# Optimization experiments

Hardware: AMD Instinct MI355X
Metric: run time of the kernel (lower is better)

Reference implementation:

```python
import jax, jax.numpy as jnp
import numpy as np

N_NODES = 50000
N_EDGES = 600000
F_IN = 128
DIM_H = 256
N_CLASSES = 40
BN_EPS = 1e-5


def setup_inputs() -> dict:
    key = jax.random.key(0)
    ks = jax.random.split(key, 10)
    x = jax.random.normal(ks[0], (N_NODES, F_IN), dtype=jnp.float32)
    edge_index = jax.random.randint(ks[1], (2, N_EDGES), 0, N_NODES, dtype=jnp.int64)
    s1 = 1.0 / np.sqrt(F_IN)
    s2 = 1.0 / np.sqrt(DIM_H)
    W1 = jax.random.uniform(ks[2], (F_IN, DIM_H), jnp.float32, -s1, s1)
    b1 = jax.random.uniform(ks[3], (DIM_H,), jnp.float32, -s1, s1)
    gamma = jnp.ones((DIM_H,), jnp.float32)
    beta = jnp.zeros((DIM_H,), jnp.float32)
    W2 = jax.random.uniform(ks[4], (DIM_H, DIM_H), jnp.float32, -s2, s2)
    b2 = jax.random.uniform(ks[5], (DIM_H,), jnp.float32, -s2, s2)
    Wlin = jax.random.uniform(ks[6], (DIM_H, N_CLASSES), jnp.float32, -s2, s2)
    blin = jax.random.uniform(ks[7], (N_CLASSES,), jnp.float32, -s2, s2)
    return {"x": x, "edge_index": edge_index, "W1": W1, "b1": b1,
            "gamma": gamma, "beta": beta, "W2": W2, "b2": b2,
            "Wlin": Wlin, "blin": blin}


def reference(x, edge_index, W1, b1, gamma, beta, W2, b2, Wlin, blin):
    src, dst = edge_index[0], edge_index[1]
    # GIN sum aggregation: agg[i] = sum_{(j->i)} x[j]; eps = 0 (default)
    agg = jax.ops.segment_sum(x[src], dst, num_segments=N_NODES)  # [N, F_IN]
    h = x + agg
    # MLP: Linear -> BatchNorm1d (training-mode batch stats) -> ReLU -> Linear -> ReLU
    h = h @ W1 + b1                               # [N, DIM_H]
    mean = jnp.mean(h, axis=0)
    var = jnp.var(h, axis=0)                      # biased, as torch BN uses for normalization
    h = (h - mean) * jax.lax.rsqrt(var + BN_EPS) * gamma + beta
    h = jax.nn.relu(h)
    h = jax.nn.relu(h @ W2 + b2)                  # MLP final ReLU; outer x.relu() is idempotent
    return h @ Wlin + blin                        # [N, N_CLASSES]
```

## Files before the change

### kernel.cpp

```cpp
#include <hip/hip_runtime.h>

#define F_IN 128
#define DIM_H 256
#define N_CLASSES 40
#define BN_EPS 1e-5f
#define M_PAD 50176

typedef short bf16x8 __attribute__((ext_vector_type(8)));
typedef float f32x4 __attribute__((ext_vector_type(4)));

__device__ __forceinline__ unsigned short f2bf(float f) {
    union { float f; unsigned u; } v; v.f = f;
    unsigned r = v.u + 0x7fff + ((v.u >> 16) & 1);
    return (unsigned short)(r >> 16);
}
__device__ __forceinline__ float bf2f(unsigned short u) {
    union { unsigned u; float f; } v; v.u = ((unsigned)u) << 16;
    return v.f;
}
__device__ __forceinline__ float4 bf2f4(ushort4 u) {
    return make_float4(bf2f(u.x), bf2f(u.y), bf2f(u.z), bf2f(u.w));
}

__global__ void hist_kernel(const int* __restrict__ dst, int* __restrict__ hist, int nE) {
    int e = blockIdx.x * blockDim.x + threadIdx.x;
    if (e >= nE) return;
    atomicAdd(&hist[dst[e]], 1);
}

__global__ void scan_blocks_kernel(const int* __restrict__ hist,
                                   int* __restrict__ blockSums, int M) {
    __shared__ int lds[256];
    int t = threadIdx.x;
    int i = blockIdx.x * 256 + t;
    lds[t] = (i < M) ? hist[i] : 0;
    __syncthreads();
    for (int off = 128; off > 0; off >>= 1) {
        if (t < off) lds[t] += lds[t + off];
        __syncthreads();
    }
    if (t == 0) blockSums[blockIdx.x] = lds[0];
}

__global__ void scan_final_kernel(const int* __restrict__ hist,
                                  const int* __restrict__ blockSums,
                                  int* __restrict__ start, int M, int nE) {
    __shared__ int lds[256];
    int t = threadIdx.x;
    lds[t] = (t < blockIdx.x) ? blockSums[t] : 0;
    __syncthreads();
    for (int o = 128; o > 0; o >>= 1) {
        if (t < o) lds[t] += lds[t + o];
        __syncthreads();
    }
    int off = lds[0];
    __syncthreads();
    int i = blockIdx.x * 256 + t;
    int orig = (i < M) ? hist[i] : 0;
    lds[t] = orig;
    __syncthreads();
    for (int o = 1; o < 256; o <<= 1) {
        int v = (t >= o) ? lds[t - o] : 0;
        __syncthreads();
        lds[t] += v;
        __syncthreads();
    }
    if (i < M) start[i] = off + lds[t] - orig;
    if (blockIdx.x == 0 && t == 0) start[M] = nE;
}

__global__ void fill_kernel(const int* __restrict__ src, const int* __restrict__ dst,
                            const int* __restrict__ start, int* __restrict__ cursor,
                            int* __restrict__ order, int nE) {
    int e = blockIdx.x * blockDim.x + threadIdx.x;
    if (e >= nE) return;
    int d = dst[e];
    int pos = start[d] + atomicAdd(&cursor[d], 1);
    order[pos] = src[e];
}

__global__ void prep_kernel(const float* __restrict__ x, unsigned short* __restrict__ xb,
                            const float* __restrict__ W1, const float* __restrict__ W2,
                            const float* __restrict__ Wl,
                            unsigned short* __restrict__ W1t,
                            unsigned short* __restrict__ W2t,
                            unsigned short* __restrict__ Wlt,
                            int* __restrict__ histz, int XQ, int ZQ) {
    int idx = blockIdx.x * 256 + threadIdx.x;
    if (idx < XQ) {
        float4 v = ((const float4*)x)[idx];
        ushort4 o;
        o.x = f2bf(v.x); o.y = f2bf(v.y); o.z = f2bf(v.z); o.w = f2bf(v.w);
        ((ushort4*)xb)[idx] = o;
        return;
    }
    int j = idx - XQ;
    if (j < 32768) {
        int n = j >> 7, k = j & 127;
        W1t[j] = f2bf(W1[k * DIM_H + n]);
    } else if (j < 32768 + 65536) {
        int i = j - 32768;
        int n = i >> 8, k = i & 255;
        W2t[i] = f2bf(W2[k * DIM_H + n]);
    } else if (j < 32768 + 65536 + 16384) {
        int i = j - 98304;
        int n = i >> 8, k = i & 255;
        Wlt[i] = f2bf((n < N_CLASSES) ? Wl[k * N_CLASSES + n] : 0.f);
    } else {
        int z = j - 114688;
        if (z >= 0 && z < ZQ) ((int4*)histz)[z] = make_int4(0, 0, 0, 0);
    }
}

__global__ void bn_reduce_kernel(const float* __restrict__ partials, int R,
                                 const float* __restrict__ gamma,
                                 const float* __restrict__ beta,
                                 float* __restrict__ scale,
                                 float* __restrict__ shift, int M) {
    __shared__ float ls[256], lss[256];
    int c = blockIdx.x, t = threadIdx.x;
    float s = 0.f, ss = 0.f;
    for (int r = t; r < R; r += 256) {
        s += partials[(long)r * 512 + c];
        ss += partials[(long)r * 512 + 256 + c];
    }
    ls[t] = s; lss[t] = ss;
    __syncthreads();
    for (int o = 128; o > 0; o >>= 1) {
        if (t < o) { ls[t] += ls[t + o]; lss[t] += lss[t + o]; }
        __syncthreads();
    }
    if (t == 0) {
        float inv = 1.0f / (float)M;
        float mean = ls[0] * inv;
        float var = lss[0] * inv - mean * mean;
        float sc = gamma[c] * rsqrtf(var + BN_EPS);
        scale[c] = sc;
        shift[c] = beta[c] - mean * sc;
    }
}

__global__ __launch_bounds__(256) void gather_kernel(
    const unsigned short* __restrict__ xb,
    const int* __restrict__ order, const int* __restrict__ start,
    unsigned short* __restrict__ A1, int M) {
    int node = blockIdx.x * 8 + (threadIdx.x >> 5);
    if (node >= M) return;
    int lane32 = threadIdx.x & 31;
    const ushort4* xv = (const ushort4*)xb;
    float4 a0 = bf2f4(xv[(size_t)node * 32 + lane32]);
    float4 a1 = make_float4(0.f, 0.f, 0.f, 0.f);
    float4 a2 = a1, a3 = a1;
    int e0 = start[node], e1 = start[node + 1];
    int e = e0;
    for (; e + 8 <= e1; e += 8) {
        int s0 = order[e],     s1 = order[e + 1], s2 = order[e + 2], s3 = order[e + 3];
        int s4 = order[e + 4], s5 = order[e + 5], s6 = order[e + 6], s7 = order[e + 7];
        ushort4 u0 = xv[(size_t)s0 * 32 + lane32];
        ushort4 u1 = xv[(size_t)s1 * 32 + lane32];
        ushort4 u2 = xv[(size_t)s2 * 32 + lane32];
        ushort4 u3 = xv[(size_t)s3 * 32 + lane32];
        ushort4 u4 = xv[(size_t)s4 * 32 + lane32];
        ushort4 u5 = xv[(size_t)s5 * 32 + lane32];
        ushort4 u6 = xv[(size_t)s6 * 32 + lane32];
        ushort4 u7 = xv[(size_t)s7 * 32 + lane32];
        float4 v0 = bf2f4(u0), v1 = bf2f4(u1), v2 = bf2f4(u2), v3 = bf2f4(u3);
        float4 v4 = bf2f4(u4), v5 = bf2f4(u5), v6 = bf2f4(u6), v7 = bf2f4(u7);
        a0.x += v0.x; a0.y += v0.y; a0.z += v0.z; a0.w += v0.w;
        a1.x += v1.x; a1.y += v1.y; a1.z += v1.z; a1.w += v1.w;
        a2.x += v2.x; a2.y += v2.y; a2.z += v2.z; a2.w += v2.w;
        a3.x += v3.x; a3.y += v3.y; a3.z += v3.z; a3.w += v3.w;
        a0.x += v4.x; a0.y += v4.y; a0.z += v4.z; a0.w += v4.w;
        a1.x += v5.x; a1.y += v5.y; a1.z += v5.z; a1.w += v5.w;
        a2.x += v6.x; a2.y += v6.y; a2.z += v6.z; a2.w += v6.w;
        a3.x += v7.x; a3.y += v7.y; a3.z += v7.z; a3.w += v7.w;
    }
    for (; e + 4 <= e1; e += 4) {
        int s0 = order[e], s1 = order[e + 1], s2 = order[e + 2], s3 = order[e + 3];
        float4 v0 = bf2f4(xv[(size_t)s0 * 32 + lane32]);
        float4 v1 = bf2f4(xv[(size_t)s1 * 32 + lane32]);
        float4 v2 = bf2f4(xv[(size_t)s2 * 32 + lane32]);
        float4 v3 = bf2f4(xv[(size_t)s3 * 32 + lane32]);
        a0.x += v0.x; a0.y += v0.y; a0.z += v0.z; a0.w += v0.w;
        a1.x += v1.x; a1.y += v1.y; a1.z += v1.z; a1.w += v1.w;
        a2.x += v2.x; a2.y += v2.y; a2.z += v2.z; a2.w += v2.w;
        a3.x += v3.x; a3.y += v3.y; a3.z += v3.z; a3.w += v3.w;
    }
    for (; e < e1; ++e) {
        float4 v = bf2f4(xv[(size_t)order[e] * 32 + lane32]);
        a1.x += v.x; a1.y += v.y; a1.z += v.z; a1.w += v.w;
    }
    float4 t;
    t.x = (a0.x + a1.x) + (a2.x + a3.x);
    t.y = (a0.y + a1.y) + (a2.y + a3.y);
    t.z = (a0.z + a1.z) + (a2.z + a3.z);
    t.w = (a0.w + a1.w) + (a2.w + a3.w);
    ushort4 o;
    o.x = f2bf(t.x); o.y = f2bf(t.y); o.z = f2bf(t.z); o.w = f2bf(t.w);
    ((ushort4*)A1)[(size_t)node * 32 + lane32] = o;
}

__global__ __launch_bounds__(512, 4) void gemm1_kernel(
    const unsigned short* __restrict__ A1, const unsigned short* __restrict__ W1t,
    const float* __restrict__ b1, unsigned short* __restrict__ h1,
    float* __restrict__ partials, int M) {
    constexpr int S = 4;
    constexpr int PA = 40, PB = 40, PH = 264;
    constexpr int STAGE = 128 * PA + 256 * PB;
    __shared__ __align__(16) unsigned short lds[128 * PH];
    unsigned short* h1t = lds;

    int tid = threadIdx.x;
    int wave = tid >> 6, lane = tid & 63;
    int wm = wave >> 2, wn = wave & 3;
    int l15 = lane & 15, q = lane >> 4;
    long row0 = (long)blockIdx.x * 128;

    int am = tid >> 2, ac = tid & 3;
    bf16x8 ar, br[2];
    auto loadAB = [&](int s) {
        ar = *(const bf16x8*)(A1 + (row0 + am) * F_IN + s * 32 + ac * 8);
#pragma unroll
        for (int i = 0; i < 2; ++i) {
            int ch = tid + i * 512;
            int m = ch >> 2, c = ch & 3;
            br[i] = *(const bf16x8*)(W1t + m * F_IN + s * 32 + c * 8);
        }
    };
    auto writeAB = [&](int buf) {
        unsigned short* As = lds + buf * STAGE;
        unsigned short* Bs = As + 128 * PA;
        *(bf16x8*)(&As[am * PA + ac * 8]) = ar;
#pragma unroll
        for (int i = 0; i < 2; ++i) {
            int ch = tid + i * 512;
            int m = ch >> 2, c = ch & 3;
            *(bf16x8*)(&Bs[m * PB + c * 8]) = br[i];
        }
    };

    f32x4 acc[4][4] = {};
    loadAB(0);
    writeAB(0);
#pragma unroll
    for (int s = 0; s < S; ++s) {
        if (s + 1 < S) loadAB(s + 1);
        __syncthreads();
        const unsigned short* As = lds + (s & 1) * STAGE;
        const unsigned short* Bs = As + 128 * PA;
        bf16x8 af[4], bfr[4];
#pragma unroll
        for (int mt = 0; mt < 4; ++mt)
            af[mt] = *(const bf16x8*)(&As[(wm * 64 + mt * 16 + l15) * PA + q * 8]);
#pragma unroll
        for (int nt = 0; nt < 4; ++nt)
            bfr[nt] = *(const bf16x8*)(&Bs[(wn * 64 + nt * 16 + l15) * PB + q * 8]);
#pragma unroll
        for (int mt = 0; mt < 4; ++mt)
#pragma unroll
            for (int nt = 0; nt < 4; ++nt)
                acc[mt][nt] = __builtin_amdgcn_mfma_f32_16x16x32_bf16(
                    af[mt], bfr[nt], acc[mt][nt], 0, 0, 0);
        if (s + 1 < S) writeAB((s + 1) & 1);
    }
    __syncthreads();

#pragma unroll
    for (int nt = 0; nt < 4; ++nt) {
        int col = wn * 64 + nt * 16 + l15;
        float b = b1[col];
        float s = 0.f, ss = 0.f;
#pragma unroll
        for (int mt = 0; mt < 4; ++mt) {
#pragma unroll
            for (int r = 0; r < 4; ++r) {
                long row = row0 + wm * 64 + mt * 16 + q * 4 + r;
                float v = acc[mt][nt][r] + b;
                if (row < M) { s += v; ss += v * v; }
                h1t[(wm * 64 + mt * 16 + q * 4 + r) * PH + col] = f2bf(v);
            }
        }
        s += __shfl_xor(s, 16, 64);  s += __shfl_xor(s, 32, 64);
        ss += __shfl_xor(ss, 16, 64); ss += __shfl_xor(ss, 32, 64);
        if (lane < 16) {
            long pr = (long)blockIdx.x * 2 + wm;
            partials[pr * 512 + col] = s;
            partials[pr * 512 + 256 + col] = ss;
        }
    }
    __syncthreads();
    {
        int srow = tid >> 2, scol = (tid & 3) * 64;
        unsigned short* dst = h1 + (row0 + srow) * DIM_H + scol;
        const unsigned short* srcp = &h1t[srow * PH + scol];
#pragma unroll
        for (int j = 0; j < 8; ++j)
            *(bf16x8*)(dst + j * 8) = *(const bf16x8*)(srcp + j * 8);
    }
}

__global__ __launch_bounds__(512, 4) void gemm23_kernel(
    const unsigned short* __restrict__ h1, const unsigned short* __restrict__ W2t,
    const float* __restrict__ b2,
    const float* __restrict__ scale, const float* __restrict__ shift,
    const unsigned short* __restrict__ Wlt, const float* __restrict__ blin,
    float* __restrict__ out, int M) {
    constexpr int S = 8;
    constexpr int PA = 40, PB = 40, PH = 264;
    constexpr int STAGE = 128 * PA + 256 * PB;
    __shared__ __align__(16) unsigned short lds[128 * PH];
    unsigned short* h2t = lds;

    int tid = threadIdx.x;
    int wave = tid >> 6, lane = tid & 63;
    int wm = wave >> 2, wn = wave & 3;
    int l15 = lane & 15, q = lane >> 4;
    long row0 = (long)blockIdx.x * 128;

    int am = tid >> 2, ac = tid & 3;
    bf16x8 ar, br[2];
    auto loadAB = [&](int s) {
        ar = *(const bf16x8*)(h1 + (row0 + am) * DIM_H + s * 32 + ac * 8);
#pragma unroll
        for (int i = 0; i < 2; ++i) {
            int ch = tid + i * 512;
            int m = ch >> 2, c = ch & 3;
            br[i] = *(const bf16x8*)(W2t + m * DIM_H + s * 32 + c * 8);
        }
    };
    auto writeAB = [&](int s, int buf) {
        unsigned short* As = lds + buf * STAGE;
        unsigned short* Bs = As + 128 * PA;
        {
            int kb = s * 32 + ac * 8;
            float4 sc0 = *(const float4*)(scale + kb);
            float4 sc1 = *(const float4*)(scale + kb + 4);
            float4 sh0 = *(const float4*)(shift + kb);
            float4 sh1 = *(const float4*)(shift + kb + 4);
            float scv[8] = {sc0.x, sc0.y, sc0.z, sc0.w, sc1.x, sc1.y, sc1.z, sc1.w};
            float shv[8] = {sh0.x, sh0.y, sh0.z, sh0.w, sh1.x, sh1.y, sh1.z, sh1.w};
            bf16x8 v = ar;
#pragma unroll
            for (int j = 0; j < 8; ++j) {
                float f = bf2f((unsigned short)v[j]);
                f = fmaxf(f * scv[j] + shv[j], 0.f);
                v[j] = (short)f2bf(f);
            }
            *(bf16x8*)(&As[am * PA + ac * 8]) = v;
        }
#pragma unroll
        for (int i = 0; i < 2; ++i) {
            int ch = tid + i * 512;
            int m = ch >> 2, c = ch & 3;
            *(bf16x8*)(&Bs[m * PB + c * 8]) = br[i];
        }
    };

    f32x4 acc[4][4] = {};
    loadAB(0);
    writeAB(0, 0);
#pragma unroll
    for (int s = 0; s < S; ++s) {
        if (s + 1 < S) loadAB(s + 1);
        __syncthreads();
        const unsigned short* As = lds + (s & 1) * STAGE;
        const unsigned short* Bs = As + 128 * PA;
        bf16x8 af[4], bfr[4];
#pragma unroll
        for (int mt = 0; mt < 4; ++mt)
            af[mt] = *(const bf16x8*)(&As[(wm * 64 + mt * 16 + l15) * PA + q * 8]);
#pragma unroll
        for (int nt = 0; nt < 4; ++nt)
            bfr[nt] = *(const bf16x8*)(&Bs[(wn * 64 + nt * 16 + l15) * PB + q * 8]);
#pragma unroll
        for (int mt = 0; mt < 4; ++mt)
#pragma unroll
            for (int nt = 0; nt < 4; ++nt)
                acc[mt][nt] = __builtin_amdgcn_mfma_f32_16x16x32_bf16(
                    af[mt], bfr[nt], acc[mt][nt], 0, 0, 0);
        if (s + 1 < S) writeAB(s + 1, (s + 1) & 1);
    }
    __syncthreads();

#pragma unroll
    for (int nt = 0; nt < 4; ++nt) {
        int colL = wn * 64 + nt * 16 + l15;
        float b = b2[colL];
#pragma unroll
        for (int mt = 0; mt < 4; ++mt)
#pragma unroll
            for (int r = 0; r < 4; ++r) {
                int rowL = wm * 64 + mt * 16 + q * 4 + r;
                h2t[rowL * PH + colL] = f2bf(fmaxf(acc[mt][nt][r] + b, 0.f));
            }
    }
    __syncthreads();

    f32x4 acc3[3] = {};
#pragma unroll
    for (int s = 0; s < 8; ++s) {
        bf16x8 a3 = *(const bf16x8*)(&h2t[(wave * 16 + l15) * PH + s * 32 + q * 8]);
#pragma unroll
        for (int nt = 0; nt < 3; ++nt) {
            bf16x8 b3 = *(const bf16x8*)(Wlt + (nt * 16 + l15) * 256 + s * 32 + q * 8);
            acc3[nt] = __builtin_amdgcn_mfma_f32_16x16x32_bf16(a3, b3, acc3[nt], 0, 0, 0);
        }
    }
#pragma unroll
    for (int nt = 0; nt < 3; ++nt) {
        int col = nt * 16 + l15;
        if (col < N_CLASSES) {
            float b = blin[col];
#pragma unroll
            for (int r = 0; r < 4; ++r) {
                long row = row0 + wave * 16 + q * 4 + r;
                if (row < M) out[row * N_CLASSES + col] = acc3[nt][r] + b;
            }
        }
    }
}

extern "C" void kernel_launch(void* const* d_in, const int* in_sizes, int n_in,
                              void* d_out, int out_size, void* d_ws, size_t ws_size,
                              hipStream_t stream) {
    const float* x     = (const float*)d_in[0];
    const int*   ei    = (const int*)d_in[1];
    const float* W1    = (const float*)d_in[2];
    const float* b1    = (const float*)d_in[3];
    const float* gamma = (const float*)d_in[4];
    const float* beta  = (const float*)d_in[5];
    const float* W2    = (const float*)d_in[6];
    const float* b2    = (const float*)d_in[7];
    const float* Wlin  = (const float*)d_in[8];
    const float* blin  = (const float*)d_in[9];
    float* out = (float*)d_out;

    int M  = in_sizes[0] / F_IN;
    int nE = in_sizes[1] / 2;
    const int* srcIdx = ei;
    const int* dstIdx = ei + nE;
    int nB = (M + 255) / 256;
    int g128 = (M + 127) / 128;
    int XQ = M * 32;
    int ZQ = 2 * M / 4;

    unsigned short* h1bf  = (unsigned short*)d_ws;
    unsigned short* xb    = h1bf + (size_t)M_PAD * DIM_H;
    unsigned short* A1bf  = xb + (size_t)M_PAD * F_IN;
    unsigned short* W1t   = A1bf + (size_t)M_PAD * F_IN;
    unsigned short* W2t   = W1t + DIM_H * F_IN;
    unsigned short* Wlt   = W2t + DIM_H * DIM_H;
    float*          partials = (float*)(Wlt + 64 * DIM_H);
    float*          scale = partials + (size_t)800 * 512;
    float*          shift = scale + DIM_H;
    int*            hist  = (int*)(shift + DIM_H);
    int*            cursor= hist + M;
    int*            start = cursor + M;
    int*            blockSums = start + (M + 1);
    int*            order = blockSums + 256;

    int tB = 256;
    prep_kernel<<<(XQ + 114688 + ZQ + 255) / 256, 256, 0, stream>>>(
        x, xb, W1, W2, Wlin, W1t, W2t, Wlt, hist, XQ, ZQ);
    hist_kernel<<<(nE + tB - 1) / tB, tB, 0, stream>>>(dstIdx, hist, nE);
    scan_blocks_kernel<<<nB, 256, 0, stream>>>(hist, blockSums, M);
    scan_final_kernel<<<nB, 256, 0, stream>>>(hist, blockSums, start, M, nE);
    fill_kernel<<<(nE + tB - 1) / tB, tB, 0, stream>>>(srcIdx, dstIdx, start, cursor, order, nE);

    gather_kernel<<<(M + 7) / 8, 256, 0, stream>>>(xb, order, start, A1bf, M);
    gemm1_kernel<<<g128, 512, 0, stream>>>(A1bf, W1t, b1, h1bf, partials, M);
    bn_reduce_kernel<<<DIM_H, 256, 0, stream>>>(partials, 2 * g128, gamma, beta, scale, shift, M);
    gemm23_kernel<<<g128, 512, 0, stream>>>(h1bf, W2t, b2, scale, shift, Wlt, blin, out, M);
}
```

Before: 233.6 us.

## Fuse BN reduction into GEMM via atomics and widen gather loads to 16 bytes

Removes the separate bn_reduce kernel. gemm1 now atomically accumulates the per-column sum and sum of squares into a zeroed global buffer, and gemm23 computes scale and shift into shared memory at startup. This saves one launch and the partials round trip, at the cost of atomic contention on 512 addresses and fp32 atomic ordering nondeterminism. Separately, the gather kernel uses 16 lanes per node with 16-byte bf16x8 loads instead of 32 lanes with 8-byte loads, and cuts the accumulators from four to two.

```diff
diff --git a/kernel.cpp b/kernel.cpp
--- a/kernel.cpp
+++ b/kernel.cpp
@@ -17,9 +17,6 @@
 __device__ __forceinline__ float bf2f(unsigned short u) {
     union { unsigned u; float f; } v; v.u = ((unsigned)u) << 16;
     return v.f;
-}
-__device__ __forceinline__ float4 bf2f4(ushort4 u) {
-    return make_float4(bf2f(u.x), bf2f(u.y), bf2f(u.z), bf2f(u.w));
 }
 
 __global__ void hist_kernel(const int* __restrict__ dst, int* __restrict__ hist, int nE) {
@@ -112,98 +109,65 @@
     }
 }
 
-__global__ void bn_reduce_kernel(const float* __restrict__ partials, int R,
-                                 const float* __restrict__ gamma,
-                                 const float* __restrict__ beta,
-                                 float* __restrict__ scale,
-                                 float* __restrict__ shift, int M) {
-    __shared__ float ls[256], lss[256];
-    int c = blockIdx.x, t = threadIdx.x;
-    float s = 0.f, ss = 0.f;
-    for (int r = t; r < R; r += 256) {
-        s += partials[(long)r * 512 + c];
-        ss += partials[(long)r * 512 + 256 + c];
-    }
-    ls[t] = s; lss[t] = ss;
-    __syncthreads();
-    for (int o = 128; o > 0; o >>= 1) {
-        if (t < o) { ls[t] += ls[t + o]; lss[t] += lss[t + o]; }
-        __syncthreads();
-    }
-    if (t == 0) {
-        float inv = 1.0f / (float)M;
-        float mean = ls[0] * inv;
-        float var = lss[0] * inv - mean * mean;
-        float sc = gamma[c] * rsqrtf(var + BN_EPS);
-        scale[c] = sc;
-        shift[c] = beta[c] - mean * sc;
-    }
-}
-
 __global__ __launch_bounds__(256) void gather_kernel(
     const unsigned short* __restrict__ xb,
     const int* __restrict__ order, const int* __restrict__ start,
     unsigned short* __restrict__ A1, int M) {
-    int node = blockIdx.x * 8 + (threadIdx.x >> 5);
+    int node = blockIdx.x * 16 + (threadIdx.x >> 4);
     if (node >= M) return;
-    int lane32 = threadIdx.x & 31;
-    const ushort4* xv = (const ushort4*)xb;
-    float4 a0 = bf2f4(xv[(size_t)node * 32 + lane32]);
-    float4 a1 = make_float4(0.f, 0.f, 0.f, 0.f);
-    float4 a2 = a1, a3 = a1;
+    int lane = threadIdx.x & 15;
+    const bf16x8* xv = (const bf16x8*)xb;
+    size_t base = (size_t)node * 16 + lane;
+    bf16x8 us = xv[base];
+    float a0[8], a1[8];
+#pragma unroll
+    for (int j = 0; j < 8; ++j) { a0[j] = bf2f((unsigned short)us[j]); a1[j] = 0.f; }
     int e0 = start[node], e1 = start[node + 1];
     int e = e0;
     for (; e + 8 <= e1; e += 8) {
         int s0 = order[e],     s1 = order[e + 1], s2 = order[e + 2], s3 = order[e + 3];
         int s4 = order[e + 4], s5 = order[e + 5], s6 = order[e + 6], s7 = order[e + 7];
-        ushort4 u0 = xv[(size_t)s0 * 32 + lane32];
-        ushort4 u1 = xv[(size_t)s1 * 32 + lane32];
-        ushort4 u2 = xv[(size_t)s2 * 32 + lane32];
-        ushort4 u3 = xv[(size_t)s3 * 32 + lane32];
-        ushort4 u4 = xv[(size_t)s4 * 32 + lane32];
-        ushort4 u5 = xv[(size_t)s5 * 32 + lane32];
-        ushort4 u6 = xv[(size_t)s6 * 32 + lane32];
-        ushort4 u7 = xv[(size_t)s7 * 32 + lane32];
-        float4 v0 = bf2f4(u0), v1 = bf2f4(u1), v2 = bf2f4(u2), v3 = bf2f4(u3);
-        float4 v4 = bf2f4(u4), v5 = bf2f4(u5), v6 = bf2f4(u6), v7 = bf2f4(u7);
-        a0.x += v0.x; a0.y += v0.y; a0.z += v0.z; a0.w += v0.w;
-        a1.x += v1.x; a1.y += v1.y; a1.z += v1.z; a1.w += v1.w;
-        a2.x += v2.x; a2.y += v2.y; a2.z += v2.z; a2.w += v2.w;
-        a3.x += v3.x; a3.y += v3.y; a3.z += v3.z; a3.w += v3.w;
-        a0.x += v4.x; a0.y += v4.y; a0.z += v4.z; a0.w += v4.w;
-        a1.x += v5.x; a1.y += v5.y; a1.z += v5.z; a1.w += v5.w;
-        a2.x += v6.x; a2.y += v6.y; a2.z += v6.z; a2.w += v6.w;
-        a3.x += v7.x; a3.y += v7.y; a3.z += v7.z; a3.w += v7.w;
-    }
-    for (; e + 4 <= e1; e += 4) {
-        int s0 = order[e], s1 = order[e + 1], s2 = order[e + 2], s3 = order[e + 3];
-        float4 v0 = bf2f4(xv[(size_t)s0 * 32 + lane32]);
-        float4 v1 = bf2f4(xv[(size_t)s1 * 32 + lane32]);
-        float4 v2 = bf2f4(xv[(size_t)s2 * 32 + lane32]);
-        float4 v3 = bf2f4(xv[(size_t)s3 * 32 + lane32]);
-        a0.x += v0.x; a0.y += v0.y; a0.z += v0.z; a0.w += v0.w;
-        a1.x += v1.x; a1.y += v1.y; a1.z += v1.z; a1.w += v1.w;
-        a2.x += v2.x; a2.y += v2.y; a2.z += v2.z; a2.w += v2.w;
-        a3.x += v3.x; a3.y += v3.y; a3.z += v3.z; a3.w += v3.w;
-    }
-    for (; e < e1; ++e) {
-        float4 v = bf2f4(xv[(size_t)order[e] * 32 + lane32]);
-        a1.x += v.x; a1.y += v.y; a1.z += v.z; a1.w += v.w;
-    }
-    float4 t;
-    t.x = (a0.x + a1.x) + (a2.x + a3.x);
-    t.y = (a0.y + a1.y) + (a2.y + a3.y);
-    t.z = (a0.z + a1.z) + (a2.z + a3.z);
-    t.w = (a0.w + a1.w) + (a2.w + a3.w);
-    ushort4 o;
-    o.x = f2bf(t.x); o.y = f2bf(t.y); o.z = f2bf(t.z); o.w = f2bf(t.w);
-    ((ushort4*)A1)[(size_t)node * 32 + lane32] = o;
+        bf16x8 u0 = xv[(size_t)s0 * 16 + lane];
+        bf16x8 u1 = xv[(size_t)s1 * 16 + lane];
+        bf16x8 u2 = xv[(size_t)s2 * 16 + lane];
+        bf16x8 u3 = xv[(size_t)s3 * 16 + lane];
+        bf16x8 u4 = xv[(size_t)s4 * 16 + lane];
+        bf16x8 u5 = xv[(size_t)s5 * 16 + lane];
+        bf16x8 u6 = xv[(size_t)s6 * 16 + lane];
+        bf16x8 u7 = xv[(size_t)s7 * 16 + lane];
+#pragma unroll
+        for (int j = 0; j < 8; ++j) {
+            a0[j] += bf2f((unsigned short)u0[j]) + bf2f((unsigned short)u2[j])
+                   + bf2f((unsigned short)u4[j]) + bf2f((unsigned short)u6[j]);
+            a1[j] += bf2f((unsigned short)u1[j]) + bf2f((unsigned short)u3[j])
+                   + bf2f((unsigned short)u5[j]) + bf2f((unsigned short)u7[j]);
+        }
+    }
+    for (; e + 2 <= e1; e += 2) {
+        int s0 = order[e], s1 = order[e + 1];
+        bf16x8 u0 = xv[(size_t)s0 * 16 + lane];
+        bf16x8 u1 = xv[(size_t)s1 * 16 + lane];
+#pragma unroll
+        for (int j = 0; j < 8; ++j) {
+            a0[j] += bf2f((unsigned short)u0[j]);
+            a1[j] += bf2f((unsigned short)u1[j]);
+        }
+    }
+    if (e < e1) {
+        bf16x8 u0 = xv[(size_t)order[e] * 16 + lane];
+#pragma unroll
+        for (int j = 0; j < 8; ++j) a0[j] += bf2f((unsigned short)u0[j]);
+    }
+    bf16x8 o;
+#pragma unroll
+    for (int j = 0; j < 8; ++j) o[j] = (short)f2bf(a0[j] + a1[j]);
+    ((bf16x8*)A1)[base] = o;
 }
 
 __global__ __launch_bounds__(512, 4) void gemm1_kernel(
     const unsigned short* __restrict__ A1, const unsigned short* __restrict__ W1t,
     const float* __restrict__ b1, unsigned short* __restrict__ h1,
-    float* __restrict__ partials, int M) {
+    float* __restrict__ bnsum, int M) {
     constexpr int S = 4;
     constexpr int PA = 40, PB = 40, PH = 264;
     constexpr int STAGE = 128 * PA + 256 * PB;
@@ -283,9 +247,8 @@
         s += __shfl_xor(s, 16, 64);  s += __shfl_xor(s, 32, 64);
         ss += __shfl_xor(ss, 16, 64); ss += __shfl_xor(ss, 32, 64);
         if (lane < 16) {
-            long pr = (long)blockIdx.x * 2 + wm;
-            partials[pr * 512 + col] = s;
-            partials[pr * 512 + 256 + col] = ss;
+            atomicAdd(&bnsum[col], s);
+            atomicAdd(&bnsum[DIM_H + col], ss);
         }
     }
     __syncthreads();
@@ -302,13 +265,16 @@
 __global__ __launch_bounds__(512, 4) void gemm23_kernel(
     const unsigned short* __restrict__ h1, const unsigned short* __restrict__ W2t,
     const float* __restrict__ b2,
-    const float* __restrict__ scale, const float* __restrict__ shift,
+    const float* __restrict__ bnsum,
+    const float* __restrict__ gamma, const float* __restrict__ beta,
     const unsigned short* __restrict__ Wlt, const float* __restrict__ blin,
     float* __restrict__ out, int M) {
     constexpr int S = 8;
     constexpr int PA = 40, PB = 40, PH = 264;
     constexpr int STAGE = 128 * PA + 256 * PB;
     __shared__ __align__(16) unsigned short lds[128 * PH];
+    __shared__ __align__(16) float s_scale[DIM_H];
+    __shared__ __align__(16) float s_shift[DIM_H];
     unsigned short* h2t = lds;
 
     int tid = threadIdx.x;
@@ -316,6 +282,15 @@
     int wm = wave >> 2, wn = wave & 3;
     int l15 = lane & 15, q = lane >> 4;
     long row0 = (long)blockIdx.x * 128;
+
+    if (tid < DIM_H) {
+        float inv = 1.0f / (float)M;
+        float mean = bnsum[tid] * inv;
+        float var  = bnsum[DIM_H + tid] * inv - mean * mean;
+        float sc = gamma[tid] * rsqrtf(var + BN_EPS);
+        s_scale[tid] = sc;
+        s_shift[tid] = beta[tid] - mean * sc;
+    }
 
     int am = tid >> 2, ac = tid & 3;
     bf16x8 ar, br[2];
@@ -333,10 +308,10 @@
         unsigned short* Bs = As + 128 * PA;
         {
             int kb = s * 32 + ac * 8;
-            float4 sc0 = *(const float4*)(scale + kb);
-            float4 sc1 = *(const float4*)(scale + kb + 4);
-            float4 sh0 = *(const float4*)(shift + kb);
-            float4 sh1 = *(const float4*)(shift + kb + 4);
+            float4 sc0 = *(const float4*)(s_scale + kb);
+            float4 sc1 = *(const float4*)(s_scale + kb + 4);
+            float4 sh0 = *(const float4*)(s_shift + kb);
+            float4 sh1 = *(const float4*)(s_shift + kb + 4);
             float scv[8] = {sc0.x, sc0.y, sc0.z, sc0.w, sc1.x, sc1.y, sc1.z, sc1.w};
             float shv[8] = {sh0.x, sh0.y, sh0.z, sh0.w, sh1.x, sh1.y, sh1.z, sh1.w};
             bf16x8 v = ar;
@@ -358,6 +333,7 @@
 
     f32x4 acc[4][4] = {};
     loadAB(0);
+    __syncthreads();
     writeAB(0, 0);
 #pragma unroll
     for (int s = 0; s < S; ++s) {
@@ -442,7 +418,7 @@
     int nB = (M + 255) / 256;
     int g128 = (M + 127) / 128;
     int XQ = M * 32;
-    int ZQ = 2 * M / 4;
+    int ZQ = (2 * M + 2 * DIM_H) / 4;
 
     unsigned short* h1bf  = (unsigned short*)d_ws;
     unsigned short* xb    = h1bf + (size_t)M_PAD * DIM_H;
@@ -450,12 +426,10 @@
     unsigned short* W1t   = A1bf + (size_t)M_PAD * F_IN;
     unsigned short* W2t   = W1t + DIM_H * F_IN;
     unsigned short* Wlt   = W2t + DIM_H * DIM_H;
-    float*          partials = (float*)(Wlt + 64 * DIM_H);
-    float*          scale = partials + (size_t)800 * 512;
-    float*          shift = scale + DIM_H;
-    int*            hist  = (int*)(shift + DIM_H);
+    int*            hist  = (int*)(Wlt + 64 * DIM_H);
     int*            cursor= hist + M;
-    int*            start = cursor + M;
+    float*          bnsum = (float*)(cursor + M);
+    int*            start = (int*)(bnsum + 2 * DIM_H);
     int*            blockSums = start + (M + 1);
     int*            order = blockSums + 256;
 
@@ -467,8 +441,7 @@
     scan_final_kernel<<<nB, 256, 0, stream>>>(hist, blockSums, start, M, nE);
     fill_kernel<<<(nE + tB - 1) / tB, tB, 0, stream>>>(srcIdx, dstIdx, start, cursor, order, nE);
 
-    gather_kernel<<<(M + 7) / 8, 256, 0, stream>>>(xb, order, start, A1bf, M);
-    gemm1_kernel<<<g128, 512, 0, stream>>>(A1bf, W1t, b1, h1bf, partials, M);
-    bn_reduce_kernel<<<DIM_H, 256, 0, stream>>>(partials, 2 * g128, gamma, beta, scale, shift, M);
-    gemm23_kernel<<<g128, 512, 0, stream>>>(h1bf, W2t, b2, scale, shift, Wlt, blin, out, M);
-}
+    gather_kernel<<<(M + 15) / 16, 256, 0, stream>>>(xb, order, start, A1bf, M);
+    gemm1_kernel<<<g128, 512, 0, stream>>>(A1bf, W1t, b1, h1bf, bnsum, M);
+    gemm23_kernel<<<g128, 512, 0, stream>>>(h1bf, W2t, b2, bnsum, gamma, beta, Wlt, blin, out, M);
+}
```

Measured after the change: 242.0 us. 3.6% more time.

## Fuse neighbor gather into GEMM1 and merge scan kernels

Applied to the files above, without the earlier changes.

The neighbor-sum gather now writes its bf16 rows straight into a swizzled LDS A-tile inside the first GEMM kernel. This removes the A1 intermediate buffer's global round trip and one kernel launch. The two scan kernels are merged into one, where each block recomputes its prefix by summing the histogram before it, and the scan seeds the cursor array so the fill kernel drops its start lookup. The cost is lower parallelism in the gather phase: only 391 blocks of 512 threads, and each thread group handles 8 rows serially. The prefix recomputation also adds redundant reads that grow with the block index.

```diff
diff --git a/kernel.cpp b/kernel.cpp
--- a/kernel.cpp
+++ b/kernel.cpp
@@ -28,34 +28,26 @@
     atomicAdd(&hist[dst[e]], 1);
 }
 
-__global__ void scan_blocks_kernel(const int* __restrict__ hist,
-                                   int* __restrict__ blockSums, int M) {
+__global__ void scan_kernel(const int* __restrict__ hist,
+                            int* __restrict__ start, int* __restrict__ cursor,
+                            int M, int nE) {
     __shared__ int lds[256];
+    __shared__ int s_prefix;
     int t = threadIdx.x;
-    int i = blockIdx.x * 256 + t;
-    lds[t] = (i < M) ? hist[i] : 0;
-    __syncthreads();
-    for (int off = 128; off > 0; off >>= 1) {
-        if (t < off) lds[t] += lds[t + off];
-        __syncthreads();
-    }
-    if (t == 0) blockSums[blockIdx.x] = lds[0];
-}
-
-__global__ void scan_final_kernel(const int* __restrict__ hist,
-                                  const int* __restrict__ blockSums,
-                                  int* __restrict__ start, int M, int nE) {
-    __shared__ int lds[256];
-    int t = threadIdx.x;
-    lds[t] = (t < blockIdx.x) ? blockSums[t] : 0;
+    int base = blockIdx.x * 256;
+    int s = 0;
+    for (int i = t; i < base; i += 256) s += hist[i];
+    lds[t] = s;
     __syncthreads();
     for (int o = 128; o > 0; o >>= 1) {
         if (t < o) lds[t] += lds[t + o];
         __syncthreads();
     }
-    int off = lds[0];
-    __syncthreads();
-    int i = blockIdx.x * 256 + t;
+    if (t == 0) s_prefix = lds[0];
+    __syncthreads();
+    int prefix = s_prefix;
+    __syncthreads();
+    int i = base + t;
     int orig = (i < M) ? hist[i] : 0;
     lds[t] = orig;
     __syncthreads();
@@ -65,17 +57,20 @@
         lds[t] += v;
         __syncthreads();
     }
-    if (i < M) start[i] = off + lds[t] - orig;
+    if (i < M) {
+        int v = prefix + lds[t] - orig;
+        start[i] = v;
+        cursor[i] = v;
+    }
     if (blockIdx.x == 0 && t == 0) start[M] = nE;
 }
 
 __global__ void fill_kernel(const int* __restrict__ src, const int* __restrict__ dst,
-                            const int* __restrict__ start, int* __restrict__ cursor,
+                            int* __restrict__ cursor,
                             int* __restrict__ order, int nE) {
     int e = blockIdx.x * blockDim.x + threadIdx.x;
     if (e >= nE) return;
-    int d = dst[e];
-    int pos = start[d] + atomicAdd(&cursor[d], 1);
+    int pos = atomicAdd(&cursor[dst[e]], 1);
     order[pos] = src[e];
 }
 
@@ -140,74 +135,16 @@
     }
 }
 
-__global__ __launch_bounds__(256) void gather_kernel(
+__global__ __launch_bounds__(512, 4) void gg1_kernel(
     const unsigned short* __restrict__ xb,
     const int* __restrict__ order, const int* __restrict__ start,
-    unsigned short* __restrict__ A1, int M) {
-    int node = blockIdx.x * 8 + (threadIdx.x >> 5);
-    if (node >= M) return;
-    int lane32 = threadIdx.x & 31;
-    const ushort4* xv = (const ushort4*)xb;
-    float4 a0 = bf2f4(xv[(size_t)node * 32 + lane32]);
-    float4 a1 = make_float4(0.f, 0.f, 0.f, 0.f);
-    float4 a2 = a1, a3 = a1;
-    int e0 = start[node], e1 = start[node + 1];
-    int e = e0;
-    for (; e + 8 <= e1; e += 8) {
-        int s0 = order[e],     s1 = order[e + 1], s2 = order[e + 2], s3 = order[e + 3];
-        int s4 = order[e + 4], s5 = order[e + 5], s6 = order[e + 6], s7 = order[e + 7];
-        ushort4 u0 = xv[(size_t)s0 * 32 + lane32];
-        ushort4 u1 = xv[(size_t)s1 * 32 + lane32];
-        ushort4 u2 = xv[(size_t)s2 * 32 + lane32];
-        ushort4 u3 = xv[(size_t)s3 * 32 + lane32];
-        ushort4 u4 = xv[(size_t)s4 * 32 + lane32];
-        ushort4 u5 = xv[(size_t)s5 * 32 + lane32];
-        ushort4 u6 = xv[(size_t)s6 * 32 + lane32];
-        ushort4 u7 = xv[(size_t)s7 * 32 + lane32];
-        float4 v0 = bf2f4(u0), v1 = bf2f4(u1), v2 = bf2f4(u2), v3 = bf2f4(u3);
-        float4 v4 = bf2f4(u4), v5 = bf2f4(u5), v6 = bf2f4(u6), v7 = bf2f4(u7);
-        a0.x += v0.x; a0.y += v0.y; a0.z += v0.z; a0.w += v0.w;
-        a1.x += v1.x; a1.y += v1.y; a1.z += v1.z; a1.w += v1.w;
-        a2.x += v2.x; a2.y += v2.y; a2.z += v2.z; a2.w += v2.w;
-        a3.x += v3.x; a3.y += v3.y; a3.z += v3.z; a3.w += v3.w;
-        a0.x += v4.x; a0.y += v4.y; a0.z += v4.z; a0.w += v4.w;
-        a1.x += v5.x; a1.y += v5.y; a1.z += v5.z; a1.w += v5.w;
-        a2.x += v6.x; a2.y += v6.y; a2.z += v6.z; a2.w += v6.w;
-        a3.x += v7.x; a3.y += v7.y; a3.z += v7.z; a3.w += v7.w;
-    }
-    for (; e + 4 <= e1; e += 4) {
-        int s0 = order[e], s1 = order[e + 1], s2 = order[e + 2], s3 = order[e + 3];
-        float4 v0 = bf2f4(xv[(size_t)s0 * 32 + lane32]);
-        float4 v1 = bf2f4(xv[(size_t)s1 * 32 + lane32]);
-        float4 v2 = bf2f4(xv[(size_t)s2 * 32 + lane32]);
-        float4 v3 = bf2f4(xv[(size_t)s3 * 32 + lane32]);
-        a0.x += v0.x; a0.y += v0.y; a0.z += v0.z; a0.w += v0.w;
-        a1.x += v1.x; a1.y += v1.y; a1.z += v1.z; a1.w += v1.w;
-        a2.x += v2.x; a2.y += v2.y; a2.z += v2.z; a2.w += v2.w;
-        a3.x += v3.x; a3.y += v3.y; a3.z += v3.z; a3.w += v3.w;
-    }
-    for (; e < e1; ++e) {
-        float4 v = bf2f4(xv[(size_t)order[e] * 32 + lane32]);
-        a1.x += v.x; a1.y += v.y; a1.z += v.z; a1.w += v.w;
-    }
-    float4 t;
-    t.x = (a0.x + a1.x) + (a2.x + a3.x);
-    t.y = (a0.y + a1.y) + (a2.y + a3.y);
-    t.z = (a0.z + a1.z) + (a2.z + a3.z);
-    t.w = (a0.w + a1.w) + (a2.w + a3.w);
-    ushort4 o;
-    o.x = f2bf(t.x); o.y = f2bf(t.y); o.z = f2bf(t.z); o.w = f2bf(t.w);
-    ((ushort4*)A1)[(size_t)node * 32 + lane32] = o;
-}
-
-__global__ __launch_bounds__(512, 4) void gemm1_kernel(
-    const unsigned short* __restrict__ A1, const unsigned short* __restrict__ W1t,
+    const unsigned short* __restrict__ W1t,
     const float* __restrict__ b1, unsigned short* __restrict__ h1,
     float* __restrict__ partials, int M) {
     constexpr int S = 4;
-    constexpr int PA = 40, PB = 40, PH = 264;
-    constexpr int STAGE = 128 * PA + 256 * PB;
-    __shared__ __align__(16) unsigned short lds[128 * PH];
+    constexpr int PB = 40, PH = 264;
+    __shared__ __align__(16) unsigned short lds[36864];
+    unsigned short* As = lds;
     unsigned short* h1t = lds;
 
     int tid = threadIdx.x;
@@ -216,10 +153,72 @@
     int l15 = lane & 15, q = lane >> 4;
     long row0 = (long)blockIdx.x * 128;
 
-    int am = tid >> 2, ac = tid & 3;
-    bf16x8 ar, br[2];
-    auto loadAB = [&](int s) {
-        ar = *(const bf16x8*)(A1 + (row0 + am) * F_IN + s * 32 + ac * 8);
+    {
+        const ushort4* xv = (const ushort4*)xb;
+        int g = tid >> 5, lane32 = tid & 31;
+        for (int it = 0; it < 8; ++it) {
+            int r = g * 8 + it;
+            long node = row0 + r;
+            unsigned short* arow = As + r * 128 + ((lane32 * 4) ^ ((r & 7) << 3));
+            if (node < M) {
+                float4 a0 = bf2f4(xv[(size_t)node * 32 + lane32]);
+                float4 a1 = make_float4(0.f, 0.f, 0.f, 0.f);
+                float4 a2 = a1, a3 = a1;
+                int e0 = start[node], e1 = start[node + 1];
+                int e = e0;
+                for (; e + 8 <= e1; e += 8) {
+                    int s0 = order[e],     s1 = order[e + 1], s2 = order[e + 2], s3 = order[e + 3];
+                    int s4 = order[e + 4], s5 = order[e + 5], s6 = order[e + 6], s7 = order[e + 7];
+                    ushort4 u0 = xv[(size_t)s0 * 32 + lane32];
+                    ushort4 u1 = xv[(size_t)s1 * 32 + lane32];
+                    ushort4 u2 = xv[(size_t)s2 * 32 + lane32];
+                    ushort4 u3 = xv[(size_t)s3 * 32 + lane32];
+                    ushort4 u4 = xv[(size_t)s4 * 32 + lane32];
+                    ushort4 u5 = xv[(size_t)s5 * 32 + lane32];
+                    ushort4 u6 = xv[(size_t)s6 * 32 + lane32];
+                    ushort4 u7 = xv[(size_t)s7 * 32 + lane32];
+                    float4 v0 = bf2f4(u0), v1 = bf2f4(u1), v2 = bf2f4(u2), v3 = bf2f4(u3);
+                    float4 v4 = bf2f4(u4), v5 = bf2f4(u5), v6 = bf2f4(u6), v7 = bf2f4(u7);
+                    a0.x += v0.x; a0.y += v0.y; a0.z += v0.z; a0.w += v0.w;
+                    a1.x += v1.x; a1.y += v1.y; a1.z += v1.z; a1.w += v1.w;
+                    a2.x += v2.x; a2.y += v2.y; a2.z += v2.z; a2.w += v2.w;
+                    a3.x += v3.x; a3.y += v3.y; a3.z += v3.z; a3.w += v3.w;
+                    a0.x += v4.x; a0.y += v4.y; a0.z += v4.z; a0.w += v4.w;
+                    a1.x += v5.x; a1.y += v5.y; a1.z += v5.z; a1.w += v5.w;
+                    a2.x += v6.x; a2.y += v6.y; a2.z += v6.z; a2.w += v6.w;
+                    a3.x += v7.x; a3.y += v7.y; a3.z += v7.z; a3.w += v7.w;
+                }
+                for (; e + 4 <= e1; e += 4) {
+                    int s0 = order[e], s1 = order[e + 1], s2 = order[e + 2], s3 = order[e + 3];
+                    float4 v0 = bf2f4(xv[(size_t)s0 * 32 + lane32]);
+                    float4 v1 = bf2f4(xv[(size_t)s1 * 32 + lane32]);
+                    float4 v2 = bf2f4(xv[(size_t)s2 * 32 + lane32]);
+                    float4 v3 = bf2f4(xv[(size_t)s3 * 32 + lane32]);
+                    a0.x += v0.x; a0.y += v0.y; a0.z += v0.z; a0.w += v0.w;
+                    a1.x += v1.x; a1.y += v1.y; a1.z += v1.z; a1.w += v1.w;
+                    a2.x += v2.x; a2.y += v2.y; a2.z += v2.z; a2.w += v2.w;
+                    a3.x += v3.x; a3.y += v3.y; a3.z += v3.z; a3.w += v3.w;
+                }
+                for (; e < e1; ++e) {
+                    float4 v = bf2f4(xv[(size_t)order[e] * 32 + lane32]);
+                    a1.x += v.x; a1.y += v.y; a1.z += v.z; a1.w += v.w;
+                }
+                float4 t;
+                t.x = (a0.x + a1.x) + (a2.x + a3.x);
+                t.y = (a0.y + a1.y) + (a2.y + a3.y);
+                t.z = (a0.z + a1.z) + (a2.z + a3.z);
+                t.w = (a0.w + a1.w) + (a2.w + a3.w);
+                ushort4 o;
+                o.x = f2bf(t.x); o.y = f2bf(t.y); o.z = f2bf(t.z); o.w = f2bf(t.w);
+                *(ushort4*)arow = o;
+            } else {
+                *(ushort4*)arow = make_ushort4(0, 0, 0, 0);
+            }
+        }
+    }
+
+    bf16x8 br[2];
+    auto loadB = [&](int s) {
 #pragma unroll
         for (int i = 0; i < 2; ++i) {
             int ch = tid + i * 512;
@@ -227,10 +226,8 @@
             br[i] = *(const bf16x8*)(W1t + m * F_IN + s * 32 + c * 8);
         }
     };
-    auto writeAB = [&](int buf) {
-        unsigned short* As = lds + buf * STAGE;
-        unsigned short* Bs = As + 128 * PA;
-        *(bf16x8*)(&As[am * PA + ac * 8]) = ar;
+    auto writeB = [&](int buf) {
+        unsigned short* Bs = lds + 16384 + buf * 10240;
 #pragma unroll
         for (int i = 0; i < 2; ++i) {
             int ch = tid + i * 512;
@@ -240,18 +237,19 @@
     };
 
     f32x4 acc[4][4] = {};
-    loadAB(0);
-    writeAB(0);
+    loadB(0);
+    writeB(0);
 #pragma unroll
     for (int s = 0; s < S; ++s) {
-        if (s + 1 < S) loadAB(s + 1);
-        __syncthreads();
-        const unsigned short* As = lds + (s & 1) * STAGE;
-        const unsigned short* Bs = As + 128 * PA;
+        if (s + 1 < S) loadB(s + 1);
+        __syncthreads();
+        const unsigned short* Bs = lds + 16384 + (s & 1) * 10240;
         bf16x8 af[4], bfr[4];
 #pragma unroll
-        for (int mt = 0; mt < 4; ++mt)
-            af[mt] = *(const bf16x8*)(&As[(wm * 64 + mt * 16 + l15) * PA + q * 8]);
+        for (int mt = 0; mt < 4; ++mt) {
+            int row = wm * 64 + mt * 16 + l15;
+            af[mt] = *(const bf16x8*)(&As[row * 128 + ((s * 32 + q * 8) ^ ((row & 7) << 3))]);
+        }
 #pragma unroll
         for (int nt = 0; nt < 4; ++nt)
             bfr[nt] = *(const bf16x8*)(&Bs[(wn * 64 + nt * 16 + l15) * PB + q * 8]);
@@ -261,7 +259,7 @@
             for (int nt = 0; nt < 4; ++nt)
                 acc[mt][nt] = __builtin_amdgcn_mfma_f32_16x16x32_bf16(
                     af[mt], bfr[nt], acc[mt][nt], 0, 0, 0);
-        if (s + 1 < S) writeAB((s + 1) & 1);
+        if (s + 1 < S) writeB((s + 1) & 1);
     }
     __syncthreads();
 
@@ -274,10 +272,11 @@
         for (int mt = 0; mt < 4; ++mt) {
 #pragma unroll
             for (int r = 0; r < 4; ++r) {
-                long row = row0 + wm * 64 + mt * 16 + q * 4 + r;
+                int rowL = wm * 64 + mt * 16 + q * 4 + r;
+                long row = row0 + rowL;
                 float v = acc[mt][nt][r] + b;
                 if (row < M) { s += v; ss += v * v; }
-                h1t[(wm * 64 + mt * 16 + q * 4 + r) * PH + col] = f2bf(v);
+                h1t[rowL * PH + col] = f2bf(v);
             }
         }
         s += __shfl_xor(s, 16, 64);  s += __shfl_xor(s, 32, 64);
@@ -442,12 +441,11 @@
     int nB = (M + 255) / 256;
     int g128 = (M + 127) / 128;
     int XQ = M * 32;
-    int ZQ = 2 * M / 4;
+    int ZQ = M / 4;
 
     unsigned short* h1bf  = (unsigned short*)d_ws;
     unsigned short* xb    = h1bf + (size_t)M_PAD * DIM_H;
-    unsigned short* A1bf  = xb + (size_t)M_PAD * F_IN;
-    unsigned short* W1t   = A1bf + (size_t)M_PAD * F_IN;
+    unsigned short* W1t   = xb + (size_t)M_PAD * F_IN;
     unsigned short* W2t   = W1t + DIM_H * F_IN;
     unsigned short* Wlt   = W2t + DIM_H * DIM_H;
     float*          partials = (float*)(Wlt + 64 * DIM_H);
@@ -456,19 +454,16 @@
     int*            hist  = (int*)(shift + DIM_H);
     int*            cursor= hist + M;
     int*            start = cursor + M;
-    int*            blockSums = start + (M + 1);
-    int*            order = blockSums + 256;
+    int*            order = start + (M + 1);
 
     int tB = 256;
     prep_kernel<<<(XQ + 114688 + ZQ + 255) / 256, 256, 0, stream>>>(
         x, xb, W1, W2, Wlin, W1t, W2t, Wlt, hist, XQ, ZQ);
     hist_kernel<<<(nE + tB - 1) / tB, tB, 0, stream>>>(dstIdx, hist, nE);
-    scan_blocks_kernel<<<nB, 256, 0, stream>>>(hist, blockSums, M);
-    scan_final_kernel<<<nB, 256, 0, stream>>>(hist, blockSums, start, M, nE);
-    fill_kernel<<<(nE + tB - 1) / tB, tB, 0, stream>>>(srcIdx, dstIdx, start, cursor, order, nE);
-
-    gather_kernel<<<(M + 7) / 8, 256, 0, stream>>>(xb, order, start, A1bf, M);
-    gemm1_kernel<<<g128, 512, 0, stream>>>(A1bf, W1t, b1, h1bf, partials, M);
+    scan_kernel<<<nB, 256, 0, stream>>>(hist, start, cursor, M, nE);
+    fill_kernel<<<(nE + tB - 1) / tB, tB, 0, stream>>>(srcIdx, dstIdx, cursor, order, nE);
+
+    gg1_kernel<<<g128, 512, 0, stream>>>(xb, order, start, W1t, b1, h1bf, partials, M);
     bn_reduce_kernel<<<DIM_H, 256, 0, stream>>>(partials, 2 * g128, gamma, beta, scale, shift, M);
     gemm23_kernel<<<g128, 512, 0, stream>>>(h1bf, W2t, b2, scale, shift, Wlt, blin, out, M);
 }
```

New measurement: 262.0 us. +12.2%, slower.

## Merge scan kernels, use atomic BN sums, fold BN finalize into gemm23

Applied to the files above, without the earlier changes.

The two-pass block scan becomes one scan kernel: each block re-reads the preceding histogram entries to compute its own prefix, and it also initialises the cursor array so the fill kernel needs only a single atomic. Per-block BatchNorm partial sums in gemm1 are replaced by float atomicAdds into a 512-entry global buffer, which is zeroed in prep. The separate bn_reduce kernel is removed, and each gemm23 block computes scale and shift into LDS itself. The goal is fewer kernel launches and less intermediate traffic. The costs are heavy atomic contention on 512 addresses, a scan that does quadratic total work over the histogram, and nondeterministic float summation order.

```diff
diff --git a/kernel.cpp b/kernel.cpp
--- a/kernel.cpp
+++ b/kernel.cpp
@@ -28,34 +28,26 @@
     atomicAdd(&hist[dst[e]], 1);
 }
 
-__global__ void scan_blocks_kernel(const int* __restrict__ hist,
-                                   int* __restrict__ blockSums, int M) {
+__global__ void scan_kernel(const int* __restrict__ hist,
+                            int* __restrict__ start, int* __restrict__ cursor,
+                            int M, int nE) {
     __shared__ int lds[256];
+    __shared__ int s_prefix;
     int t = threadIdx.x;
-    int i = blockIdx.x * 256 + t;
-    lds[t] = (i < M) ? hist[i] : 0;
-    __syncthreads();
-    for (int off = 128; off > 0; off >>= 1) {
-        if (t < off) lds[t] += lds[t + off];
-        __syncthreads();
-    }
-    if (t == 0) blockSums[blockIdx.x] = lds[0];
-}
-
-__global__ void scan_final_kernel(const int* __restrict__ hist,
-                                  const int* __restrict__ blockSums,
-                                  int* __restrict__ start, int M, int nE) {
-    __shared__ int lds[256];
-    int t = threadIdx.x;
-    lds[t] = (t < blockIdx.x) ? blockSums[t] : 0;
+    int base = blockIdx.x * 256;
+    int s = 0;
+    for (int i = t; i < base; i += 256) s += hist[i];
+    lds[t] = s;
     __syncthreads();
     for (int o = 128; o > 0; o >>= 1) {
         if (t < o) lds[t] += lds[t + o];
         __syncthreads();
     }
-    int off = lds[0];
-    __syncthreads();
-    int i = blockIdx.x * 256 + t;
+    if (t == 0) s_prefix = lds[0];
+    __syncthreads();
+    int prefix = s_prefix;
+    __syncthreads();
+    int i = base + t;
     int orig = (i < M) ? hist[i] : 0;
     lds[t] = orig;
     __syncthreads();
@@ -65,17 +57,20 @@
         lds[t] += v;
         __syncthreads();
     }
-    if (i < M) start[i] = off + lds[t] - orig;
+    if (i < M) {
+        int v = prefix + lds[t] - orig;
+        start[i] = v;
+        cursor[i] = v;
+    }
     if (blockIdx.x == 0 && t == 0) start[M] = nE;
 }
 
 __global__ void fill_kernel(const int* __restrict__ src, const int* __restrict__ dst,
-                            const int* __restrict__ start, int* __restrict__ cursor,
+                            int* __restrict__ cursor,
                             int* __restrict__ order, int nE) {
     int e = blockIdx.x * blockDim.x + threadIdx.x;
     if (e >= nE) return;
-    int d = dst[e];
-    int pos = start[d] + atomicAdd(&cursor[d], 1);
+    int pos = atomicAdd(&cursor[dst[e]], 1);
     order[pos] = src[e];
 }
 
@@ -109,34 +104,6 @@
     } else {
         int z = j - 114688;
         if (z >= 0 && z < ZQ) ((int4*)histz)[z] = make_int4(0, 0, 0, 0);
-    }
-}
-
-__global__ void bn_reduce_kernel(const float* __restrict__ partials, int R,
-                                 const float* __restrict__ gamma,
-                                 const float* __restrict__ beta,
-                                 float* __restrict__ scale,
-                                 float* __restrict__ shift, int M) {
-    __shared__ float ls[256], lss[256];
-    int c = blockIdx.x, t = threadIdx.x;
-    float s = 0.f, ss = 0.f;
-    for (int r = t; r < R; r += 256) {
-        s += partials[(long)r * 512 + c];
-        ss += partials[(long)r * 512 + 256 + c];
-    }
-    ls[t] = s; lss[t] = ss;
-    __syncthreads();
-    for (int o = 128; o > 0; o >>= 1) {
-        if (t < o) { ls[t] += ls[t + o]; lss[t] += lss[t + o]; }
-        __syncthreads();
-    }
-    if (t == 0) {
-        float inv = 1.0f / (float)M;
-        float mean = ls[0] * inv;
-        float var = lss[0] * inv - mean * mean;
-        float sc = gamma[c] * rsqrtf(var + BN_EPS);
-        scale[c] = sc;
-        shift[c] = beta[c] - mean * sc;
     }
 }
 
@@ -203,7 +170,7 @@
 __global__ __launch_bounds__(512, 4) void gemm1_kernel(
     const unsigned short* __restrict__ A1, const unsigned short* __restrict__ W1t,
     const float* __restrict__ b1, unsigned short* __restrict__ h1,
-    float* __restrict__ partials, int M) {
+    float* __restrict__ bnsum, int M) {
     constexpr int S = 4;
     constexpr int PA = 40, PB = 40, PH = 264;
     constexpr int STAGE = 128 * PA + 256 * PB;
@@ -283,9 +250,8 @@
         s += __shfl_xor(s, 16, 64);  s += __shfl_xor(s, 32, 64);
         ss += __shfl_xor(ss, 16, 64); ss += __shfl_xor(ss, 32, 64);
         if (lane < 16) {
-            long pr = (long)blockIdx.x * 2 + wm;
-            partials[pr * 512 + col] = s;
-            partials[pr * 512 + 256 + col] = ss;
+            atomicAdd(&bnsum[col], s);
+            atomicAdd(&bnsum[DIM_H + col], ss);
         }
     }
     __syncthreads();
@@ -302,13 +268,16 @@
 __global__ __launch_bounds__(512, 4) void gemm23_kernel(
     const unsigned short* __restrict__ h1, const unsigned short* __restrict__ W2t,
     const float* __restrict__ b2,
-    const float* __restrict__ scale, const float* __restrict__ shift,
+    const float* __restrict__ bnsum,
+    const float* __restrict__ gamma, const float* __restrict__ beta,
     const unsigned short* __restrict__ Wlt, const float* __restrict__ blin,
     float* __restrict__ out, int M) {
     constexpr int S = 8;
     constexpr int PA = 40, PB = 40, PH = 264;
     constexpr int STAGE = 128 * PA + 256 * PB;
     __shared__ __align__(16) unsigned short lds[128 * PH];
+    __shared__ __align__(16) float s_scale[DIM_H];
+    __shared__ __align__(16) float s_shift[DIM_H];
     unsigned short* h2t = lds;
 
     int tid = threadIdx.x;
@@ -316,6 +285,15 @@
     int wm = wave >> 2, wn = wave & 3;
     int l15 = lane & 15, q = lane >> 4;
     long row0 = (long)blockIdx.x * 128;
+
+    if (tid < DIM_H) {
+        float inv = 1.0f / (float)M;
+        float mean = bnsum[tid] * inv;
+        float var  = bnsum[DIM_H + tid] * inv - mean * mean;
+        float sc = gamma[tid] * rsqrtf(var + BN_EPS);
+        s_scale[tid] = sc;
+        s_shift[tid] = beta[tid] - mean * sc;
+    }
 
     int am = tid >> 2, ac = tid & 3;
     bf16x8 ar, br[2];
@@ -333,10 +311,10 @@
         unsigned short* Bs = As + 128 * PA;
         {
             int kb = s * 32 + ac * 8;
-            float4 sc0 = *(const float4*)(scale + kb);
-            float4 sc1 = *(const float4*)(scale + kb + 4);
-            float4 sh0 = *(const float4*)(shift + kb);
-            float4 sh1 = *(const float4*)(shift + kb + 4);
+            float4 sc0 = *(const float4*)(s_scale + kb);
+            float4 sc1 = *(const float4*)(s_scale + kb + 4);
+            float4 sh0 = *(const float4*)(s_shift + kb);
+            float4 sh1 = *(const float4*)(s_shift + kb + 4);
             float scv[8] = {sc0.x, sc0.y, sc0.z, sc0.w, sc1.x, sc1.y, sc1.z, sc1.w};
             float shv[8] = {sh0.x, sh0.y, sh0.z, sh0.w, sh1.x, sh1.y, sh1.z, sh1.w};
             bf16x8 v = ar;
@@ -358,6 +336,7 @@
 
     f32x4 acc[4][4] = {};
     loadAB(0);
+    __syncthreads();
     writeAB(0, 0);
 #pragma unroll
     for (int s = 0; s < S; ++s) {
@@ -442,7 +421,7 @@
     int nB = (M + 255) / 256;
     int g128 = (M + 127) / 128;
     int XQ = M * 32;
-    int ZQ = 2 * M / 4;
+    int ZQ = (M + 2 * DIM_H) / 4;
 
     unsigned short* h1bf  = (unsigned short*)d_ws;
     unsigned short* xb    = h1bf + (size_t)M_PAD * DIM_H;
@@ -450,25 +429,21 @@
     unsigned short* W1t   = A1bf + (size_t)M_PAD * F_IN;
     unsigned short* W2t   = W1t + DIM_H * F_IN;
     unsigned short* Wlt   = W2t + DIM_H * DIM_H;
-    float*          partials = (float*)(Wlt + 64 * DIM_H);
-    float*          scale = partials + (size_t)800 * 512;
-    float*          shift = scale + DIM_H;
-    int*            hist  = (int*)(shift + DIM_H);
-    int*            cursor= hist + M;
+    int*            hist  = (int*)(Wlt + 64 * DIM_H);
+    float*          bnsum = (float*)(hist + M);
+    int*            cursor= (int*)(bnsum + 2 * DIM_H);
     int*            start = cursor + M;
-    int*            blockSums = start + (M + 1);
-    int*            order = blockSums + 256;
+    int*            order = start + (M + 1);
 
     int tB = 256;
     prep_kernel<<<(XQ + 114688 + ZQ + 255) / 256, 256, 0, stream>>>(
         x, xb, W1, W2, Wlin, W1t, W2t, Wlt, hist, XQ, ZQ);
     hist_kernel<<<(nE + tB - 1) / tB, tB, 0, stream>>>(dstIdx, hist, nE);
-    scan_blocks_kernel<<<nB, 256, 0, stream>>>(hist, blockSums, M);
-    scan_final_kernel<<<nB, 256, 0, stream>>>(hist, blockSums, start, M, nE);
-    fill_kernel<<<(nE + tB - 1) / tB, tB, 0, stream>>>(srcIdx, dstIdx, start, cursor, order, nE);
+    scan_kernel<<<nB, 256, 0, stream>>>(hist, start, cursor, M, nE);
+    fill_kernel<<<(nE + tB - 1) / tB, tB, 0, stream>>>(srcIdx, dstIdx, cursor, order, nE);
 
     gather_kernel<<<(M + 7) / 8, 256, 0, stream>>>(xb, order, start, A1bf, M);
-    gemm1_kernel<<<g128, 512, 0, stream>>>(A1bf, W1t, b1, h1bf, partials, M);
-    bn_reduce_kernel<<<DIM_H, 256, 0, stream>>>(partials, 2 * g128, gamma, beta, scale, shift, M);
-    gemm23_kernel<<<g128, 512, 0, stream>>>(h1bf, W2t, b2, scale, shift, Wlt, blin, out, M);
-}
+    gemm1_kernel<<<g128, 512, 0, stream>>>(A1bf, W1t, b1, h1bf, bnsum, M);
+    gemm23_kernel<<<g128, 512, 0, stream>>>(h1bf, W2t, b2, bnsum, gamma, beta,
+                                            Wlt, blin, out, M);
+}
```

After: 263.5 us. +12.8%, slower.
